# Optimization experiments

Hardware: AMD Instinct MI355X
Metric: run time of the kernel (lower is better)

Reference implementation:

```python
import jax, jax.numpy as jnp
import numpy as np

# QTIP QuantizedLinear config (decode_mode='lut')
IN_F, OUT_F = 4096, 4096
TD_X, TD_Y = 16, 16          # weight tile
L, K, V = 16, 2, 2           # trellis state bits, bits/weight, values/state
TLUT_BITS = 16               # lut mode: tlut_bits == L


def fwht(x):
    """Normalized fast Walsh-Hadamard transform over the last axis (power of 2).
    Equivalent to matmul_hadU with K=1 (features are powers of two)."""
    n = x.shape[-1]
    h = 1
    while h < n:
        x = x.reshape(x.shape[:-1] + (n // (2 * h), 2, h))
        a, b = x[..., 0, :], x[..., 1, :]
        x = jnp.stack([a + b, a - b], axis=-2).reshape(x.shape[:-3] + (n,))
        h *= 2
    return x / jnp.sqrt(jnp.float32(n))


def dequantize_weight(trellis, tlut):
    """Bitshift trellis decode: each 16x16 tile stores td_x*td_y*K = 512 bits.
    The stream is walked KV = K*V bits per step (tail-biting); each L-bit state
    indexes the LUT producing V weights. trellis holds uint16 words in int32."""
    num_tiles = trellis.shape[0]
    T = TD_X * TD_Y            # 256 weights per tile
    S = T // V                 # 128 trellis steps per tile
    KV = K * V                 # 4 fresh bits per step
    steps = L // KV            # 4 nibbles form one L-bit state
    words = trellis & 0xFFFF
    bit_pos = jnp.arange(15, -1, -1)                     # MSB-first within word
    bits = (words[:, :, None] >> bit_pos) & 1            # (tiles, 32, 16)
    nib_w = 2 ** jnp.arange(KV - 1, -1, -1)
    nibs = jnp.sum(bits.reshape(num_tiles, S, KV) * nib_w, axis=-1)  # (tiles, S)
    # state_i = (nib[i-3]<<12)|(nib[i-2]<<8)|(nib[i-1]<<4)|nib[i], wraparound (tail-biting)
    states = jnp.zeros_like(nibs)
    for j in range(steps):
        states = states | (jnp.roll(nibs, j, axis=1) << (KV * j))
    vals = tlut[states]                                  # (tiles, S, V)
    W = vals.reshape(OUT_F // TD_X, IN_F // TD_Y, TD_X, TD_Y)
    return W.transpose(0, 2, 1, 3).reshape(OUT_F, IN_F)


def setup_inputs() -> dict:
    key = jax.random.key(0)
    k1, k2, k3, k4, k5 = jax.random.split(key, 5)
    inp = jax.random.normal(k1, (8, 2048, IN_F), jnp.float32)
    num_tiles = (OUT_F // TD_X) * (IN_F // TD_Y)
    words = (TD_X * TD_Y * K + 15) // 16
    trellis = jax.random.randint(k2, (num_tiles, words), 0, 65536, jnp.int32)
    tlut = jax.random.normal(k3, (2 ** TLUT_BITS, V), jnp.float32)
    SU = jax.random.normal(k4, (IN_F,), jnp.float32)
    SV = jax.random.normal(k5, (OUT_F,), jnp.float32)
    return {"input": inp, "trellis": trellis, "tlut": tlut, "SU": SU, "SV": SV}


def reference(input, trellis, tlut, SU, SV):
    W = dequantize_weight(trellis, tlut)          # (OUT_F, IN_F)
    x = input.reshape(-1, IN_F) * SU              # input rescale (sign vector)
    x = fwht(x)                                   # left Hadamard rotation
    x = x @ W.T                                   # fused dequant matmul
    x = fwht(x)                                   # right Hadamard rotation
    x = x * SV                                    # output rescale
    return x.reshape(input.shape[:-1] + (OUT_F,))
```

## Files before the change

### kernel.cpp

```cpp
#include <hip/hip_runtime.h>

typedef __attribute__((ext_vector_type(8))) short short8;
typedef __attribute__((ext_vector_type(4))) float f32x4;

__device__ __forceinline__ unsigned short f2bf(float f) {
  union { float f; unsigned u; } x{f};
  unsigned r = x.u + 0x7FFFu + ((x.u >> 16) & 1u);
  return (unsigned short)(r >> 16);
}

__device__ __forceinline__ void gload_lds16(const void* g, void* l) {
  __builtin_amdgcn_global_load_lds(
      (__attribute__((address_space(1))) void*)((unsigned long long)g),
      (__attribute__((address_space(3))) void*)(unsigned)((unsigned long long)l),
      16, 0, 0);
}

__global__ void k_dequant(const int* __restrict__ trellis,
                          const float* __restrict__ tlut,
                          float* __restrict__ W) {
  __shared__ unsigned short words[64];
  const int t = threadIdx.x;
  if (t < 64) words[t] = (unsigned short)(trellis[(size_t)blockIdx.x * 64 + t] & 0xFFFF);
  __syncthreads();
  const int tl = t >> 7;
  const int s  = t & 127;
  const unsigned short* w = &words[tl * 32];
  unsigned state = 0;
#pragma unroll
  for (int j = 0; j < 4; ++j) {
    const int ss = (s - j) & 127;
    const unsigned nb = ((unsigned)w[ss >> 2] >> (12 - 4 * (ss & 3))) & 0xFu;
    state |= nb << (4 * j);
  }
  const float2 v = *(const float2*)(tlut + (size_t)state * 2);
  const int tile = blockIdx.x * 2 + tl;
  const int o = ((tile >> 8) << 4) + (s >> 3);
  const int i = ((tile & 255) << 4) + ((s & 7) << 1);
  *(float2*)(W + (size_t)o * 4096 + i) = v;
}

__global__ void k_fwht_row(float* __restrict__ W) {
  __shared__ float row[4096];
  const int t = threadIdx.x;
  float* g = W + ((size_t)blockIdx.x << 12);
#pragma unroll
  for (int k = 0; k < 4; ++k) {
    const int e = (t + (k << 8)) << 2;
    *(float4*)(row + e) = *(const float4*)(g + e);
  }
  __syncthreads();
  for (int h = 1; h < 4096; h <<= 1) {
#pragma unroll
    for (int k = 0; k < 8; ++k) {
      const int p  = t + (k << 8);
      const int j1 = ((p & ~(h - 1)) << 1) | (p & (h - 1));
      const int j2 = j1 + h;
      const float a = row[j1], b = row[j2];
      row[j1] = a + b;
      row[j2] = a - b;
    }
    __syncthreads();
  }
#pragma unroll
  for (int k = 0; k < 4; ++k) {
    const int e = (t + (k << 8)) << 2;
    float4 v = *(float4*)(row + e);
    v.x *= 0.015625f; v.y *= 0.015625f; v.z *= 0.015625f; v.w *= 0.015625f;
    *(float4*)(g + e) = v;
  }
}

__device__ __forceinline__ void butterfly64(float (*tile)[64], int t) {
  const int c  = t & 63;
  const int pb = t >> 6;
#pragma unroll
  for (int h = 1; h < 64; h <<= 1) {
#pragma unroll
    for (int k = 0; k < 8; ++k) {
      const int p  = pb + (k << 2);
      const int j1 = ((p & ~(h - 1)) << 1) | (p & (h - 1));
      const int j2 = j1 + h;
      const float a = tile[j1][c], b = tile[j2][c];
      tile[j1][c] = a + b;
      tile[j2][c] = a - b;
    }
    __syncthreads();
  }
}

__global__ void k_fwht_col1(float* __restrict__ W) {
  __shared__ float tile[64][64];
  const int t  = threadIdx.x;
  const int rg = blockIdx.x >> 6;
  const int cg = blockIdx.x & 63;
  const size_t base = ((size_t)rg << 6) * 4096 + ((size_t)cg << 6);
#pragma unroll
  for (int k = 0; k < 4; ++k) {
    const int idx = t + (k << 8);
    const int r = idx >> 4, c4 = idx & 15;
    *(float4*)(&tile[r][c4 << 2]) = *(const float4*)(W + base + (size_t)r * 4096 + (c4 << 2));
  }
  __syncthreads();
  butterfly64(tile, t);
#pragma unroll
  for (int k = 0; k < 4; ++k) {
    const int idx = t + (k << 8);
    const int r = idx >> 4, c4 = idx & 15;
    *(float4*)(W + base + (size_t)r * 4096 + (c4 << 2)) = *(float4*)(&tile[r][c4 << 2]);
  }
}

__global__ void k_fwht_col2(const float* __restrict__ W,
                            const float* __restrict__ SU,
                            const float* __restrict__ SV,
                            unsigned short* __restrict__ Mt) {
  __shared__ float tile[64][64];
  const int t  = threadIdx.x;
  const int b  = blockIdx.x >> 6;
  const int cg = blockIdx.x & 63;
#pragma unroll
  for (int k = 0; k < 4; ++k) {
    const int idx = t + (k << 8);
    const int a = idx >> 4, c4 = idx & 15;
    const int row = (a << 6) + b;
    *(float4*)(&tile[a][c4 << 2]) =
        *(const float4*)(W + (size_t)row * 4096 + ((size_t)cg << 6) + (c4 << 2));
  }
  __syncthreads();
  butterfly64(tile, t);
#pragma unroll
  for (int k = 0; k < 4; ++k) {
    const int idx = t + (k << 8);
    const int a = idx >> 4, c4 = idx & 15;
    const int row = (a << 6) + b;
    const int col0 = (cg << 6) + (c4 << 2);
    const float sv = SV[row] * 0.015625f;
    const float4 su = *(const float4*)(SU + col0);
    const float4 v = *(float4*)(&tile[a][c4 << 2]);
    ushort4 o;
    o.x = f2bf(v.x * sv * su.x);
    o.y = f2bf(v.y * sv * su.y);
    o.z = f2bf(v.z * sv * su.z);
    o.w = f2bf(v.w * sv * su.w);
    *(ushort4*)(Mt + (size_t)row * 4096 + col0) = o;
  }
}

__global__ void k_cvt_x(const float* __restrict__ x, unsigned short* __restrict__ xb) {
  const long long n4 = (long long)16384 * 4096 / 4;
  long long i = (long long)blockIdx.x * blockDim.x + threadIdx.x;
  const long long stride = (long long)gridDim.x * blockDim.x;
  for (; i < n4; i += stride) {
    const float4 v = *(const float4*)(x + i * 4);
    ushort4 o;
    o.x = f2bf(v.x); o.y = f2bf(v.y); o.z = f2bf(v.z); o.w = f2bf(v.w);
    *(ushort4*)(xb + i * 4) = o;
  }
}

#define BARRIER __builtin_amdgcn_s_barrier()
#define SB0     __builtin_amdgcn_sched_barrier(0)
#define WAITV4  asm volatile("s_waitcnt vmcnt(4)" ::: "memory")
#define WAITV0  asm volatile("s_waitcnt vmcnt(0)" ::: "memory")
#define WAITL0  asm volatile("s_waitcnt lgkmcnt(0)" ::: "memory")

#define STAGE_A(db, h, jj) do { \
  gload_lds16(aRow + (((size_t)((h)*128      )) << 12) + ((jj) << 6), smem +         (db)*32768 + (h)*16384 +        w1k); \
  gload_lds16(aRow + (((size_t)((h)*128 + 64 )) << 12) + ((jj) << 6), smem +         (db)*32768 + (h)*16384 + 8192 + w1k); \
} while (0)
#define STAGE_B(db, h, jj) do { \
  gload_lds16(bRow + (((size_t)((h)*128      )) << 12) + ((jj) << 6), smem + 65536 + (db)*32768 + (h)*16384 +        w1k); \
  gload_lds16(bRow + (((size_t)((h)*128 + 64 )) << 12) + ((jj) << 6), smem + 65536 + (db)*32768 + (h)*16384 + 8192 + w1k); \
} while (0)

#define RD_A(kk, base, cx) do { _Pragma("unroll") \
  for (int mi = 0; mi < 8; ++mi) af[mi][kk] = *(const short8*)((base) + mi*2048 + (cx)); } while (0)
#define RD_B(kk, base, cx) do { _Pragma("unroll") \
  for (int ni = 0; ni < 4; ++ni) bb[ni][kk] = *(const short8*)((base) + ni*2048 + (cx)); } while (0)

#define MMA(nA, nB, kk) do { _Pragma("unroll") \
  for (int mi = 0; mi < 8; ++mi) { \
    acc[mi][nA] = __builtin_amdgcn_mfma_f32_16x16x32_bf16(af[mi][kk], bb[nA][kk], acc[mi][nA], 0, 0, 0); \
    acc[mi][nB] = __builtin_amdgcn_mfma_f32_16x16x32_bf16(af[mi][kk], bb[nB][kk], acc[mi][nB], 0, 0, 0); \
  } } while (0)

#define PHASE(READS, STAGE, WAIT, MMAC) do { \
  READS; STAGE; WAIT; \
  BARRIER; WAITL0; SB0; \
  __builtin_amdgcn_s_setprio(1); MMAC; __builtin_amdgcn_s_setprio(0); \
  BARRIER; SB0; \
} while (0)

__global__ void __launch_bounds__(512, 2)
k_gemm8(const unsigned short* __restrict__ A,
        const unsigned short* __restrict__ B,
        float* __restrict__ C) {
  extern __shared__ char smem[];
  const int t    = threadIdx.x;
  const int lane = t & 63, w = t >> 6;
  const int wr   = w >> 2, wc = w & 3;
  const int hb   = wc >> 1, rb = (wc & 1) * 64;
  const int lr   = lane & 15, q = lane >> 4;
  const int w1k  = w * 1024;

  const int nt = blockIdx.x & 15;
  const int mt = blockIdx.x >> 4;

  const int cx0 = lr * 128 + (((0 + q) ^ (lr & 7)) << 4);
  const int cx1 = lr * 128 + (((4 + q) ^ (lr & 7)) << 4);

  const char* As0 = smem +         wr * 16384;
  const char* As1 = smem + 32768 + wr * 16384;
  const char* Bs0 = smem + 65536 +         hb * 16384 + rb * 128;
  const char* Bs1 = smem + 65536 + 32768 + hb * 16384 + rb * 128;

  const int srow  = t >> 3;
  const int csrc8 = (((t & 7) ^ (srow & 7)) << 3);
  const unsigned short* aRow = A + (((size_t)(mt * 256 + srow)) << 12) + csrc8;
  const unsigned short* bRow = B + (((size_t)(nt * 256 + srow)) << 12) + csrc8;

  short8 af[8][2], bb[4][2];
  f32x4  acc[8][4];
#pragma unroll
  for (int i = 0; i < 8; ++i)
#pragma unroll
    for (int j = 0; j < 4; ++j) acc[i][j] = (f32x4){0.f, 0.f, 0.f, 0.f};

  STAGE_A(0, 0, 0); STAGE_A(0, 1, 0); STAGE_B(0, 0, 0); STAGE_B(0, 1, 0);
  STAGE_A(1, 0, 1); STAGE_A(1, 1, 1);
  WAITV4;
  BARRIER; SB0;

  for (int g = 0; g < 31; ++g) {
    const int j1 = 2 * g + 1, j2 = 2 * g + 2, j3 = 2 * g + 3;
    PHASE({ RD_A(0, As0, cx0); RD_B(0, Bs0, cx0); }, STAGE_B(1, 0, j1), , MMA(0, 1, 0));
    PHASE({ RD_A(1, As0, cx1); },                    STAGE_B(1, 1, j1), , MMA(2, 3, 0));
    PHASE({ RD_B(1, Bs0, cx1); },                    STAGE_A(0, 0, j2), , MMA(0, 1, 1));
    PHASE({ },                                       STAGE_A(0, 1, j2), WAITV4, MMA(2, 3, 1));
    PHASE({ RD_A(0, As1, cx0); RD_B(0, Bs1, cx0); }, STAGE_B(0, 0, j2), , MMA(0, 1, 0));
    PHASE({ RD_A(1, As1, cx1); },                    STAGE_B(0, 1, j2), , MMA(2, 3, 0));
    PHASE({ RD_B(1, Bs1, cx1); },                    STAGE_A(1, 0, j3), , MMA(0, 1, 1));
    PHASE({ },                                       STAGE_A(1, 1, j3), WAITV4, MMA(2, 3, 1));
  }
  PHASE({ RD_A(0, As0, cx0); RD_B(0, Bs0, cx0); }, STAGE_B(1, 0, 63), , MMA(0, 1, 0));
  PHASE({ RD_A(1, As0, cx1); },                    STAGE_B(1, 1, 63), , MMA(2, 3, 0));
  PHASE({ RD_B(1, Bs0, cx1); },                    ,                   , MMA(0, 1, 1));
  PHASE({ },                                       ,                   WAITV0, MMA(2, 3, 1));
  PHASE({ RD_A(0, As1, cx0); RD_B(0, Bs1, cx0); }, ,                   , MMA(0, 1, 0));
  PHASE({ RD_A(1, As1, cx1); },                    ,                   , MMA(2, 3, 0));
  PHASE({ RD_B(1, Bs1, cx1); },                    ,                   , MMA(0, 1, 1));
  PHASE({ },                                       ,                   , MMA(2, 3, 1));

  float* cbase = C + (((size_t)(mt * 256 + wr * 128 + q * 4)) << 12)
               + nt * 256 + wc * 64 + lr;
#pragma unroll
  for (int mi = 0; mi < 8; ++mi)
#pragma unroll
    for (int ni = 0; ni < 4; ++ni)
#pragma unroll
      for (int r = 0; r < 4; ++r)
        cbase[(((size_t)(mi * 16 + r)) << 12) + ni * 16] = acc[mi][ni][r];
}

extern "C" void kernel_launch(void* const* d_in, const int* in_sizes, int n_in,
                              void* d_out, int out_size, void* d_ws, size_t ws_size,
                              hipStream_t stream) {
  const float* x       = (const float*)d_in[0];
  const int*   trellis = (const int*)d_in[1];
  const float* tlut    = (const float*)d_in[2];
  const float* SU      = (const float*)d_in[3];
  const float* SV      = (const float*)d_in[4];
  float* out = (float*)d_out;

  char* ws = (char*)d_ws;
  float*          W  = (float*)ws;
  unsigned short* Mt = (unsigned short*)(ws + (64ull << 20));
  unsigned short* xb = (unsigned short*)(ws + (96ull << 20));

  hipFuncSetAttribute(reinterpret_cast<const void*>(&k_gemm8),
                      hipFuncAttributeMaxDynamicSharedMemorySize, 131072);

  hipLaunchKernelGGL(k_dequant,   dim3(32768), dim3(256), 0, stream, trellis, tlut, W);
  hipLaunchKernelGGL(k_fwht_row,  dim3(4096),  dim3(256), 0, stream, W);
  hipLaunchKernelGGL(k_fwht_col1, dim3(4096),  dim3(256), 0, stream, W);
  hipLaunchKernelGGL(k_fwht_col2, dim3(4096),  dim3(256), 0, stream, W, SU, SV, Mt);
  hipLaunchKernelGGL(k_cvt_x,     dim3(2048),  dim3(256), 0, stream, x, xb);
  hipLaunchKernelGGL(k_gemm8,     dim3(1024),  dim3(512), 131072, stream, xb, Mt, out);
}
```

Baseline: 642.8 us.

## Fuse trellis dequant with first column Hadamard pass; relax GEMM scheduling barriers

Trellis decoding and the first 64-point column butterfly now run in one kernel that decodes a 64x64 tile straight into shared memory. This removes one full write and read of the 64 MB fp32 weight buffer and one launch. Separately, the GEMM phases drop the explicit lgkmcnt waits and sched_barriers and issue B fragment reads before A. That hands LDS-wait placement to the compiler, which may shift MFMA/LDS overlap in either direction.

```diff
diff --git a/kernel.cpp b/kernel.cpp
--- a/kernel.cpp
+++ b/kernel.cpp
@@ -16,28 +16,66 @@
       16, 0, 0);
 }
 
-__global__ void k_dequant(const int* __restrict__ trellis,
-                          const float* __restrict__ tlut,
-                          float* __restrict__ W) {
-  __shared__ unsigned short words[64];
-  const int t = threadIdx.x;
-  if (t < 64) words[t] = (unsigned short)(trellis[(size_t)blockIdx.x * 64 + t] & 0xFFFF);
-  __syncthreads();
-  const int tl = t >> 7;
-  const int s  = t & 127;
-  const unsigned short* w = &words[tl * 32];
-  unsigned state = 0;
-#pragma unroll
-  for (int j = 0; j < 4; ++j) {
-    const int ss = (s - j) & 127;
-    const unsigned nb = ((unsigned)w[ss >> 2] >> (12 - 4 * (ss & 3))) & 0xFu;
-    state |= nb << (4 * j);
-  }
-  const float2 v = *(const float2*)(tlut + (size_t)state * 2);
-  const int tile = blockIdx.x * 2 + tl;
-  const int o = ((tile >> 8) << 4) + (s >> 3);
-  const int i = ((tile & 255) << 4) + ((s & 7) << 1);
-  *(float2*)(W + (size_t)o * 4096 + i) = v;
+__device__ __forceinline__ void butterfly64(float (*tile)[64], int t) {
+  const int c  = t & 63;
+  const int pb = t >> 6;
+#pragma unroll
+  for (int h = 1; h < 64; h <<= 1) {
+#pragma unroll
+    for (int k = 0; k < 8; ++k) {
+      const int p  = pb + (k << 2);
+      const int j1 = ((p & ~(h - 1)) << 1) | (p & (h - 1));
+      const int j2 = j1 + h;
+      const float a = tile[j1][c], b = tile[j2][c];
+      tile[j1][c] = a + b;
+      tile[j2][c] = a - b;
+    }
+    __syncthreads();
+  }
+}
+
+__global__ void k_deq_col1(const int* __restrict__ trellis,
+                           const float* __restrict__ tlut,
+                           float* __restrict__ W) {
+  __shared__ unsigned short words[16][32];
+  __shared__ float tile[64][64];
+  const int t  = threadIdx.x;
+  const int rg = blockIdx.x >> 6;
+  const int cg = blockIdx.x & 63;
+#pragma unroll
+  for (int r = 0; r < 2; ++r) {
+    const int ff = t + (r << 8);
+    const int a = ff >> 7, rw = ff & 127;
+    const int src = ((rg * 4 + a) * 256 + cg * 4) * 32 + rw;
+    ((unsigned short*)words)[a * 128 + rw] = (unsigned short)(trellis[src] & 0xFFFF);
+  }
+  __syncthreads();
+#pragma unroll
+  for (int r = 0; r < 8; ++r) {
+    const int f  = t + (r << 8);
+    const int tl = f >> 7, s = f & 127;
+    const unsigned short* w = words[tl];
+    unsigned state = 0;
+#pragma unroll
+    for (int j = 0; j < 4; ++j) {
+      const int ss = (s - j) & 127;
+      state |= (((unsigned)w[ss >> 2] >> (12 - 4 * (ss & 3))) & 0xFu) << (4 * j);
+    }
+    const float2 v = *(const float2*)(tlut + (size_t)state * 2);
+    const int o = ((tl >> 2) << 4) + (s >> 3);
+    const int i = ((tl & 3) << 4) + ((s & 7) << 1);
+    tile[o][i]     = v.x;
+    tile[o][i + 1] = v.y;
+  }
+  __syncthreads();
+  butterfly64(tile, t);
+  const size_t base = ((size_t)(rg * 64)) * 4096 + cg * 64;
+#pragma unroll
+  for (int k = 0; k < 4; ++k) {
+    const int idx = t + (k << 8);
+    const int r = idx >> 4, c4 = idx & 15;
+    *(float4*)(W + base + (size_t)r * 4096 + (c4 << 2)) = *(float4*)(&tile[r][c4 << 2]);
+  }
 }
 
 __global__ void k_fwht_row(float* __restrict__ W) {
@@ -68,46 +106,6 @@
     float4 v = *(float4*)(row + e);
     v.x *= 0.015625f; v.y *= 0.015625f; v.z *= 0.015625f; v.w *= 0.015625f;
     *(float4*)(g + e) = v;
-  }
-}
-
-__device__ __forceinline__ void butterfly64(float (*tile)[64], int t) {
-  const int c  = t & 63;
-  const int pb = t >> 6;
-#pragma unroll
-  for (int h = 1; h < 64; h <<= 1) {
-#pragma unroll
-    for (int k = 0; k < 8; ++k) {
-      const int p  = pb + (k << 2);
-      const int j1 = ((p & ~(h - 1)) << 1) | (p & (h - 1));
-      const int j2 = j1 + h;
-      const float a = tile[j1][c], b = tile[j2][c];
-      tile[j1][c] = a + b;
-      tile[j2][c] = a - b;
-    }
-    __syncthreads();
-  }
-}
-
-__global__ void k_fwht_col1(float* __restrict__ W) {
-  __shared__ float tile[64][64];
-  const int t  = threadIdx.x;
-  const int rg = blockIdx.x >> 6;
-  const int cg = blockIdx.x & 63;
-  const size_t base = ((size_t)rg << 6) * 4096 + ((size_t)cg << 6);
-#pragma unroll
-  for (int k = 0; k < 4; ++k) {
-    const int idx = t + (k << 8);
-    const int r = idx >> 4, c4 = idx & 15;
-    *(float4*)(&tile[r][c4 << 2]) = *(const float4*)(W + base + (size_t)r * 4096 + (c4 << 2));
-  }
-  __syncthreads();
-  butterfly64(tile, t);
-#pragma unroll
-  for (int k = 0; k < 4; ++k) {
-    const int idx = t + (k << 8);
-    const int r = idx >> 4, c4 = idx & 15;
-    *(float4*)(W + base + (size_t)r * 4096 + (c4 << 2)) = *(float4*)(&tile[r][c4 << 2]);
   }
 }
 
@@ -160,10 +158,8 @@
 }
 
 #define BARRIER __builtin_amdgcn_s_barrier()
-#define SB0     __builtin_amdgcn_sched_barrier(0)
 #define WAITV4  asm volatile("s_waitcnt vmcnt(4)" ::: "memory")
 #define WAITV0  asm volatile("s_waitcnt vmcnt(0)" ::: "memory")
-#define WAITL0  asm volatile("s_waitcnt lgkmcnt(0)" ::: "memory")
 
 #define STAGE_A(db, h, jj) do { \
   gload_lds16(aRow + (((size_t)((h)*128      )) << 12) + ((jj) << 6), smem +         (db)*32768 + (h)*16384 +        w1k); \
@@ -187,9 +183,9 @@
 
 #define PHASE(READS, STAGE, WAIT, MMAC) do { \
   READS; STAGE; WAIT; \
-  BARRIER; WAITL0; SB0; \
+  BARRIER; \
   __builtin_amdgcn_s_setprio(1); MMAC; __builtin_amdgcn_s_setprio(0); \
-  BARRIER; SB0; \
+  BARRIER; \
 } while (0)
 
 __global__ void __launch_bounds__(512, 2)
@@ -230,24 +226,24 @@
   STAGE_A(0, 0, 0); STAGE_A(0, 1, 0); STAGE_B(0, 0, 0); STAGE_B(0, 1, 0);
   STAGE_A(1, 0, 1); STAGE_A(1, 1, 1);
   WAITV4;
-  BARRIER; SB0;
+  BARRIER;
 
   for (int g = 0; g < 31; ++g) {
     const int j1 = 2 * g + 1, j2 = 2 * g + 2, j3 = 2 * g + 3;
-    PHASE({ RD_A(0, As0, cx0); RD_B(0, Bs0, cx0); }, STAGE_B(1, 0, j1), , MMA(0, 1, 0));
+    PHASE({ RD_B(0, Bs0, cx0); RD_A(0, As0, cx0); }, STAGE_B(1, 0, j1), , MMA(0, 1, 0));
     PHASE({ RD_A(1, As0, cx1); },                    STAGE_B(1, 1, j1), , MMA(2, 3, 0));
     PHASE({ RD_B(1, Bs0, cx1); },                    STAGE_A(0, 0, j2), , MMA(0, 1, 1));
     PHASE({ },                                       STAGE_A(0, 1, j2), WAITV4, MMA(2, 3, 1));
-    PHASE({ RD_A(0, As1, cx0); RD_B(0, Bs1, cx0); }, STAGE_B(0, 0, j2), , MMA(0, 1, 0));
+    PHASE({ RD_B(0, Bs1, cx0); RD_A(0, As1, cx0); }, STAGE_B(0, 0, j2), , MMA(0, 1, 0));
     PHASE({ RD_A(1, As1, cx1); },                    STAGE_B(0, 1, j2), , MMA(2, 3, 0));
     PHASE({ RD_B(1, Bs1, cx1); },                    STAGE_A(1, 0, j3), , MMA(0, 1, 1));
     PHASE({ },                                       STAGE_A(1, 1, j3), WAITV4, MMA(2, 3, 1));
   }
-  PHASE({ RD_A(0, As0, cx0); RD_B(0, Bs0, cx0); }, STAGE_B(1, 0, 63), , MMA(0, 1, 0));
+  PHASE({ RD_B(0, Bs0, cx0); RD_A(0, As0, cx0); }, STAGE_B(1, 0, 63), , MMA(0, 1, 0));
   PHASE({ RD_A(1, As0, cx1); },                    STAGE_B(1, 1, 63), , MMA(2, 3, 0));
   PHASE({ RD_B(1, Bs0, cx1); },                    ,                   , MMA(0, 1, 1));
   PHASE({ },                                       ,                   WAITV0, MMA(2, 3, 1));
-  PHASE({ RD_A(0, As1, cx0); RD_B(0, Bs1, cx0); }, ,                   , MMA(0, 1, 0));
+  PHASE({ RD_B(0, Bs1, cx0); RD_A(0, As1, cx0); }, ,                   , MMA(0, 1, 0));
   PHASE({ RD_A(1, As1, cx1); },                    ,                   , MMA(2, 3, 0));
   PHASE({ RD_B(1, Bs1, cx1); },                    ,                   , MMA(0, 1, 1));
   PHASE({ },                                       ,                   , MMA(2, 3, 1));
@@ -281,9 +277,8 @@
   hipFuncSetAttribute(reinterpret_cast<const void*>(&k_gemm8),
                       hipFuncAttributeMaxDynamicSharedMemorySize, 131072);
 
-  hipLaunchKernelGGL(k_dequant,   dim3(32768), dim3(256), 0, stream, trellis, tlut, W);
+  hipLaunchKernelGGL(k_deq_col1,  dim3(4096),  dim3(256), 0, stream, trellis, tlut, W);
   hipLaunchKernelGGL(k_fwht_row,  dim3(4096),  dim3(256), 0, stream, W);
-  hipLaunchKernelGGL(k_fwht_col1, dim3(4096),  dim3(256), 0, stream, W);
   hipLaunchKernelGGL(k_fwht_col2, dim3(4096),  dim3(256), 0, stream, W, SU, SV, Mt);
   hipLaunchKernelGGL(k_cvt_x,     dim3(2048),  dim3(256), 0, stream, x, xb);
   hipLaunchKernelGGL(k_gemm8,     dim3(1024),  dim3(512), 131072, stream, xb, Mt, out);
```

After: 614.1 us. -4.5%, faster.
